# Kernel tuning notes

Measured on AMD Instinct MI355X. Metric: run time of the kernel, lower is better.

The kernel has to match this reference:

```python
import jax, jax.numpy as jnp
import numpy as np

N_HEAD = 16
NEG_BIG = 1e10  # matches the module's -10000000000.0 masking constant


def setup_inputs() -> dict:
    key = jax.random.key(0)
    k1, k2, k3 = jax.random.split(key, 3)
    B, S, D = 2, 2048, 1024
    std = 0.02
    return {
        "x": jax.random.normal(k1, (B, S, D), dtype=jnp.float32),
        "c_attn_w": jax.random.normal(k2, (D, 3 * D), dtype=jnp.float32) * std,
        "c_attn_b": jnp.zeros((3 * D,), dtype=jnp.float32),
        "c_proj_w": jax.random.normal(k3, (D, D), dtype=jnp.float32) * std,
        "c_proj_b": jnp.zeros((D,), dtype=jnp.float32),
    }


def reference(x, c_attn_w, c_attn_b, c_proj_w, c_proj_b):
    B, S, D = x.shape
    H = N_HEAD
    Dh = D // H

    # c_attn: fused QKV projection (Conv1D == linear)
    qkv = jnp.einsum("bsd,df->bsf", x, c_attn_w) + c_attn_b  # [B,S,3D]
    q, k, v = jnp.split(qkv, 3, axis=-1)

    def split_heads(t):  # [B,S,D] -> [B,H,S,Dh]
        return t.reshape(B, S, H, Dh).transpose(0, 2, 1, 3)

    q, k, v = split_heads(q), split_heads(k), split_heads(v)
    present = jnp.stack([k, v], axis=1)  # [B,2,H,S,Dh]

    # scores: explicit O(S^2) matrix, scaled by sqrt(head_dim)
    w = jnp.einsum("bhqd,bhkd->bhqk", q, k) / jnp.sqrt(
        jnp.asarray(Dh, dtype=q.dtype)
    )  # [B,H,S,S]

    # causal mask, applied exactly as in the source: w*mask - 1e10*(1-mask)
    mask = jnp.tril(jnp.ones((S, S), dtype=w.dtype))[None, None]  # [1,1,S,S]
    w = w * mask - NEG_BIG * (1.0 - mask)

    w = jax.nn.softmax(w, axis=-1)
    a = jnp.einsum("bhqk,bhkd->bhqd", w, v)  # [B,H,S,Dh]

    # merge heads: [B,H,S,Dh] -> [B,S,D]
    a = a.transpose(0, 2, 1, 3).reshape(B, S, D)

    # output projection
    a = jnp.einsum("bsd,df->bsf", a, c_proj_w) + c_proj_b
    return (a, present)
```

## Files before the change

kernel.cpp:

```cpp
#include <hip/hip_runtime.h>
#include <hip/hip_bf16.h>
#include <stdint.h>

typedef __bf16 bf16_t;
typedef __bf16 bf16x8 __attribute__((ext_vector_type(8)));
typedef __bf16 bf16x4v __attribute__((ext_vector_type(4)));
typedef float f32x4 __attribute__((ext_vector_type(4)));

#define MFMA16(A, B, C) __builtin_amdgcn_mfma_f32_16x16x32_bf16((A), (B), (C), 0, 0, 0)

#define BB 2
#define SS 2048
#define DD 1024
#define HH 16
#define DH 64
#define MM (BB * SS)

__device__ __forceinline__ void load_lds16(const void* g, void* l) {
  __builtin_amdgcn_global_load_lds(
      (const __attribute__((address_space(1))) void*)g,
      (__attribute__((address_space(3))) void*)l, 16, 0, 0);
}


__global__ __launch_bounds__(256) void cvt_f32_to_bf16(const float* __restrict__ in,
                                                       bf16_t* __restrict__ out, int n4) {
  int i = blockIdx.x * blockDim.x + threadIdx.x;
  if (i >= n4) return;
  float4 v = reinterpret_cast<const float4*>(in)[i];
  bf16x4v o;
  o[0] = (bf16_t)v.x; o[1] = (bf16_t)v.y; o[2] = (bf16_t)v.z; o[3] = (bf16_t)v.w;
  reinterpret_cast<bf16x4v*>(out)[i] = o;
}

__global__ void transpose_f32_to_bf16(const float* __restrict__ W, bf16_t* __restrict__ WT,
                                      int K, int N) {
  __shared__ float tile[32][33];
  int n0 = blockIdx.x * 32, k0 = blockIdx.y * 32;
  int tx = threadIdx.x, ty = threadIdx.y;
  #pragma unroll
  for (int i = ty; i < 32; i += 8) tile[i][tx] = W[(size_t)(k0 + i) * N + n0 + tx];
  __syncthreads();
  #pragma unroll
  for (int i = ty; i < 32; i += 8) WT[(size_t)(n0 + i) * K + k0 + tx] = (bf16_t)tile[tx][i];
}

template <int EPI>
__global__ __launch_bounds__(256) void gemm_bf16(
    const bf16_t* __restrict__ A, const bf16_t* __restrict__ BT,
    const float* __restrict__ bias, float* __restrict__ outf,
    bf16_t* __restrict__ q_b, bf16_t* __restrict__ k_b, bf16_t* __restrict__ vt_b,
    int M, int N, int K) {
  __shared__ __align__(16) bf16_t At[128 * 32];
  __shared__ __align__(16) bf16_t Bt[128 * 32];

  const int tid = threadIdx.x;
  const int l = tid & 63, w = tid >> 6;
  const int lr = l & 15, lg = l >> 4;
  const int wr = w >> 1, wc = w & 1;
  const int row0 = blockIdx.y * 128, col0 = blockIdx.x * 128;

  f32x4 vz = {0.f, 0.f, 0.f, 0.f};
  f32x4 acc[4][4];
  #pragma unroll
  for (int m = 0; m < 4; ++m)
    #pragma unroll
    for (int n = 0; n < 4; ++n) acc[m][n] = vz;

  for (int k0 = 0; k0 < K; k0 += 32) {
    __syncthreads();
    #pragma unroll
    for (int i = 0; i < 2; ++i) {
      int e = (tid + i * 256) * 8;
      int r = e >> 5, c = e & 31;
      int base = (w * 64 + i * 256) * 8;
      load_lds16(&A[(size_t)(row0 + r) * K + k0 + c], &At[base]);
      load_lds16(&BT[(size_t)(col0 + r) * K + k0 + c], &Bt[base]);
    }
    __syncthreads();
    bf16x8 af[4], bfr[4];
    #pragma unroll
    for (int m = 0; m < 4; ++m)
      af[m] = *(const bf16x8*)&At[(wr * 64 + m * 16 + lr) * 32 + lg * 8];
    #pragma unroll
    for (int n = 0; n < 4; ++n)
      bfr[n] = *(const bf16x8*)&Bt[(wc * 64 + n * 16 + lr) * 32 + lg * 8];
    #pragma unroll
    for (int m = 0; m < 4; ++m)
      #pragma unroll
      for (int n = 0; n < 4; ++n) acc[m][n] = MFMA16(af[m], bfr[n], acc[m][n]);
  }

  #pragma unroll
  for (int m = 0; m < 4; ++m) {
    int rl = wr * 64 + m * 16 + lg * 4;
    #pragma unroll
    for (int n = 0; n < 4; ++n) {
      int col = col0 + wc * 64 + n * 16 + lr;
      float bz = bias[col];
      #pragma unroll
      for (int r = 0; r < 4; ++r) {
        int row = row0 + rl + r;
        float v = acc[m][n][r] + bz;
        if (EPI == 1) {
          outf[(size_t)row * N + col] = v;
        } else {
          int b = row >> 11, s = row & 2047;
          int part = col >> 10, d = col & 1023;
          int h = d >> 6, dh = d & 63;
          size_t idx = ((size_t)(b * HH + h) * SS + s) * DH + dh;
          if (part == 0) {
            q_b[idx] = (bf16_t)v;
          } else if (part == 1) {
            k_b[idx] = (bf16_t)v;
            outf[(((size_t)(b * 2 + 0) * HH + h) * SS + s) * DH + dh] = v;
          } else {
            vt_b[((size_t)(b * HH + h) * DH + dh) * SS + s] = (bf16_t)v;
            outf[(((size_t)(b * 2 + 1) * HH + h) * SS + s) * DH + dh] = v;
          }
        }
      }
    }
  }
}

__global__ __launch_bounds__(256) void attn_fwd(
    const bf16_t* __restrict__ q_b, const bf16_t* __restrict__ k_b,
    const bf16_t* __restrict__ vt_b, bf16_t* __restrict__ attn_out) {
  __shared__ __align__(16) bf16_t Kt[64 * 64];
  __shared__ __align__(16) bf16_t Vt[64 * 64];
  __shared__ __align__(16) bf16_t P_lds[4][32][72];

  const int bh = blockIdx.y;
  const int q0b = (gridDim.x - 1 - blockIdx.x) * 128;
  const int tid = threadIdx.x;
  const int w = tid >> 6, l = tid & 63;
  const int lr = l & 15, lg = l >> 4;

  const bf16_t* qb = q_b + (size_t)bh * SS * DH;
  const bf16_t* kb = k_b + (size_t)bh * SS * DH;
  const bf16_t* vt = vt_b + (size_t)bh * DH * SS;

  const int qrow0 = q0b + w * 32 + lr;
  const int qrow1 = qrow0 + 16;
  bf16x8 qf[2][2];
  qf[0][0] = *(const bf16x8*)&qb[(size_t)qrow0 * DH + lg * 8];
  qf[0][1] = *(const bf16x8*)&qb[(size_t)qrow0 * DH + 32 + lg * 8];
  qf[1][0] = *(const bf16x8*)&qb[(size_t)qrow1 * DH + lg * 8];
  qf[1][1] = *(const bf16x8*)&qb[(size_t)qrow1 * DH + 32 + lg * 8];

  f32x4 vzero = {0.f, 0.f, 0.f, 0.f};
  f32x4 oacc[2][4];
  #pragma unroll
  for (int q = 0; q < 2; ++q)
    #pragma unroll
    for (int d = 0; d < 4; ++d) oacc[q][d] = vzero;
  float m_run[2] = {-1e30f, -1e30f}, l_run[2] = {0.f, 0.f};

  const int nkv = q0b / 64 + 2;
  for (int t = 0; t < nkv; ++t) {
    const int kv0 = t * 64;
    #pragma unroll
    for (int i = 0; i < 2; ++i) {
      int e = (tid + i * 256) * 8;
      int r = e >> 6;
      int cs = (((e & 63) * 2) ^ ((r & 7) << 4)) >> 1;
      int base = (w * 64 + i * 256) * 8;
      load_lds16(&kb[(size_t)(kv0 + r) * DH + cs], &Kt[base]);
      load_lds16(&vt[(size_t)r * SS + kv0 + cs], &Vt[base]);
    }
    __syncthreads();

    float sc[2][4][4];
    #pragma unroll
    for (int kvf = 0; kvf < 4; ++kvf) {
      int rr = kvf * 16 + lr;
      int sw = (rr & 7) << 4;
      bf16x8 kf0 = *(const bf16x8*)((const char*)Kt + rr * 128 + ((lg * 16) ^ sw));
      bf16x8 kf1 = *(const bf16x8*)((const char*)Kt + rr * 128 + ((64 + lg * 16) ^ sw));
      #pragma unroll
      for (int q = 0; q < 2; ++q) {
        f32x4 a = vzero;
        a = MFMA16(kf0, qf[q][0], a);
        a = MFMA16(kf1, qf[q][1], a);
        int qrow = q ? qrow1 : qrow0;
        #pragma unroll
        for (int r = 0; r < 4; ++r) {
          int kv = kv0 + kvf * 16 + lg * 4 + r;
          float s = a[r] * 0.125f;
          sc[q][kvf][r] = (kv > qrow) ? -1e10f : s;
        }
      }
    }

    #pragma unroll
    for (int q = 0; q < 2; ++q) {
      float tmax = -1e30f;
      #pragma unroll
      for (int kvf = 0; kvf < 4; ++kvf)
        #pragma unroll
        for (int r = 0; r < 4; ++r) tmax = fmaxf(tmax, sc[q][kvf][r]);
      tmax = fmaxf(tmax, __shfl_xor(tmax, 16));
      tmax = fmaxf(tmax, __shfl_xor(tmax, 32));
      float mnew = fmaxf(m_run[q], tmax);
      float alpha = __expf(m_run[q] - mnew);
      float psum = 0.f;
      #pragma unroll
      for (int kvf = 0; kvf < 4; ++kvf)
        #pragma unroll
        for (int r = 0; r < 4; ++r) {
          float p = __expf(sc[q][kvf][r] - mnew);
          sc[q][kvf][r] = p;
          psum += p;
        }
      psum += __shfl_xor(psum, 16);
      psum += __shfl_xor(psum, 32);
      l_run[q] = l_run[q] * alpha + psum;
      m_run[q] = mnew;
      #pragma unroll
      for (int d = 0; d < 4; ++d) oacc[q][d] *= alpha;
      #pragma unroll
      for (int kvf = 0; kvf < 4; ++kvf) {
        bf16x4v pk;
        #pragma unroll
        for (int r = 0; r < 4; ++r) pk[r] = (bf16_t)sc[q][kvf][r];
        *(bf16x4v*)&P_lds[w][q * 16 + lr][kvf * 16 + lg * 4] = pk;
      }
    }

    bf16x8 pf[2][2];
    #pragma unroll
    for (int q = 0; q < 2; ++q) {
      pf[q][0] = *(const bf16x8*)&P_lds[w][q * 16 + lr][lg * 8];
      pf[q][1] = *(const bf16x8*)&P_lds[w][q * 16 + lr][32 + lg * 8];
    }
    #pragma unroll
    for (int d = 0; d < 4; ++d) {
      int dl = d * 16 + lr;
      int sw = (dl & 7) << 4;
      bf16x8 vf0 = *(const bf16x8*)((const char*)Vt + dl * 128 + ((lg * 16) ^ sw));
      bf16x8 vf1 = *(const bf16x8*)((const char*)Vt + dl * 128 + ((64 + lg * 16) ^ sw));
      #pragma unroll
      for (int q = 0; q < 2; ++q) {
        oacc[q][d] = MFMA16(vf0, pf[q][0], oacc[q][d]);
        oacc[q][d] = MFMA16(vf1, pf[q][1], oacc[q][d]);
      }
    }
    __syncthreads();
  }

  const int b = bh >> 4, h = bh & 15;
  #pragma unroll
  for (int q = 0; q < 2; ++q) {
    float inv_l = 1.f / l_run[q];
    int qrow = q ? qrow1 : qrow0;
    #pragma unroll
    for (int d = 0; d < 4; ++d)
      #pragma unroll
      for (int r = 0; r < 4; ++r) {
        int dd = d * 16 + lg * 4 + r;
        attn_out[((size_t)(b * SS + qrow)) * DD + h * DH + dd] =
            (bf16_t)(oacc[q][d][r] * inv_l);
      }
  }
}

extern "C" void kernel_launch(void* const* d_in, const int* in_sizes, int n_in,
                              void* d_out, int out_size, void* d_ws, size_t ws_size,
                              hipStream_t stream) {
  const float* x = (const float*)d_in[0];
  const float* c_attn_w = (const float*)d_in[1];
  const float* c_attn_b = (const float*)d_in[2];
  const float* c_proj_w = (const float*)d_in[3];
  const float* c_proj_b = (const float*)d_in[4];

  float* out = (float*)d_out;
  float* present = out + (size_t)BB * SS * DD;

  char* ws = (char*)d_ws;
  bf16_t* xb     = (bf16_t*)(ws + 0);
  bf16_t* wqkvT  = (bf16_t*)(ws + 8388608);
  bf16_t* wprojT = (bf16_t*)(ws + 14680064);
  bf16_t* q_b    = (bf16_t*)(ws + 16777216);
  bf16_t* k_b    = (bf16_t*)(ws + 25165824);
  bf16_t* vt_b   = (bf16_t*)(ws + 33554432);
  bf16_t* attn_o = (bf16_t*)(ws + 41943040);

  cvt_f32_to_bf16<<<(MM * DD / 4 + 255) / 256, 256, 0, stream>>>(x, xb, MM * DD / 4);
  transpose_f32_to_bf16<<<dim3(3 * DD / 32, DD / 32), dim3(32, 8), 0, stream>>>(
      c_attn_w, wqkvT, DD, 3 * DD);
  transpose_f32_to_bf16<<<dim3(DD / 32, DD / 32), dim3(32, 8), 0, stream>>>(
      c_proj_w, wprojT, DD, DD);
  gemm_bf16<0><<<dim3(3 * DD / 128, MM / 128), 256, 0, stream>>>(
      xb, wqkvT, c_attn_b, present, q_b, k_b, vt_b, MM, 3 * DD, DD);
  attn_fwd<<<dim3(SS / 128, BB * HH), 256, 0, stream>>>(q_b, k_b, vt_b, attn_o);
  gemm_bf16<1><<<dim3(DD / 128, MM / 128), 256, 0, stream>>>(
      attn_o, wprojT, c_proj_b, out, nullptr, nullptr, nullptr, MM, DD, DD);
}
```

Measured before the change: 246.2 us.

## Double-buffer LDS tiles in GEMM and attention, skip masks and lazy softmax rescale

Both the GEMM and the attention kernel now use two LDS buffers, so the next K/V or A/B tile is fetched with global_load_lds while the current one is consumed. The aim is to hide global-load latency and drop one barrier per iteration. The attention kernel also applies the causal mask only on tiles that cross the diagonal, folds log2(e) into the score scale so it can use exp2f, and skips the running-max rescale when the max grows by at most 8. The lazy rescale can let exponentials reach up to 2^8, which costs some bf16 precision in P, and doubling LDS may lower occupancy.

```diff
diff --git a/kernel.cpp b/kernel.cpp
--- a/kernel.cpp
+++ b/kernel.cpp
@@ -51,8 +51,8 @@
     const float* __restrict__ bias, float* __restrict__ outf,
     bf16_t* __restrict__ q_b, bf16_t* __restrict__ k_b, bf16_t* __restrict__ vt_b,
     int M, int N, int K) {
-  __shared__ __align__(16) bf16_t At[128 * 32];
-  __shared__ __align__(16) bf16_t Bt[128 * 32];
+  __shared__ __align__(16) bf16_t At[2][128 * 32];
+  __shared__ __align__(16) bf16_t Bt[2][128 * 32];
 
   const int tid = threadIdx.x;
   const int l = tid & 63, w = tid >> 6;
@@ -60,35 +60,42 @@
   const int wr = w >> 1, wc = w & 1;
   const int row0 = blockIdx.y * 128, col0 = blockIdx.x * 128;
 
-  f32x4 vz = {0.f, 0.f, 0.f, 0.f};
-  f32x4 acc[4][4];
-  #pragma unroll
-  for (int m = 0; m < 4; ++m)
-    #pragma unroll
-    for (int n = 0; n < 4; ++n) acc[m][n] = vz;
-
-  for (int k0 = 0; k0 < K; k0 += 32) {
-    __syncthreads();
+  auto stage = [&](int buf, int k0) {
     #pragma unroll
     for (int i = 0; i < 2; ++i) {
       int e = (tid + i * 256) * 8;
       int r = e >> 5, c = e & 31;
       int base = (w * 64 + i * 256) * 8;
-      load_lds16(&A[(size_t)(row0 + r) * K + k0 + c], &At[base]);
-      load_lds16(&BT[(size_t)(col0 + r) * K + k0 + c], &Bt[base]);
-    }
+      load_lds16(&A[(size_t)(row0 + r) * K + k0 + c], &At[buf][base]);
+      load_lds16(&BT[(size_t)(col0 + r) * K + k0 + c], &Bt[buf][base]);
+    }
+  };
+
+  f32x4 vz = {0.f, 0.f, 0.f, 0.f};
+  f32x4 acc[4][4];
+  #pragma unroll
+  for (int m = 0; m < 4; ++m)
+    #pragma unroll
+    for (int n = 0; n < 4; ++n) acc[m][n] = vz;
+
+  stage(0, 0);
+  __syncthreads();
+  int cur = 0;
+  for (int k0 = 0; k0 < K; k0 += 32) {
+    if (k0 + 32 < K) stage(cur ^ 1, k0 + 32);
+    bf16x8 af[4], bfr[4];
+    #pragma unroll
+    for (int m = 0; m < 4; ++m)
+      af[m] = *(const bf16x8*)&At[cur][(wr * 64 + m * 16 + lr) * 32 + lg * 8];
+    #pragma unroll
+    for (int n = 0; n < 4; ++n)
+      bfr[n] = *(const bf16x8*)&Bt[cur][(wc * 64 + n * 16 + lr) * 32 + lg * 8];
+    #pragma unroll
+    for (int m = 0; m < 4; ++m)
+      #pragma unroll
+      for (int n = 0; n < 4; ++n) acc[m][n] = MFMA16(af[m], bfr[n], acc[m][n]);
     __syncthreads();
-    bf16x8 af[4], bfr[4];
-    #pragma unroll
-    for (int m = 0; m < 4; ++m)
-      af[m] = *(const bf16x8*)&At[(wr * 64 + m * 16 + lr) * 32 + lg * 8];
-    #pragma unroll
-    for (int n = 0; n < 4; ++n)
-      bfr[n] = *(const bf16x8*)&Bt[(wc * 64 + n * 16 + lr) * 32 + lg * 8];
-    #pragma unroll
-    for (int m = 0; m < 4; ++m)
-      #pragma unroll
-      for (int n = 0; n < 4; ++n) acc[m][n] = MFMA16(af[m], bfr[n], acc[m][n]);
+    cur ^= 1;
   }
 
   #pragma unroll
@@ -127,8 +134,8 @@
 __global__ __launch_bounds__(256) void attn_fwd(
     const bf16_t* __restrict__ q_b, const bf16_t* __restrict__ k_b,
     const bf16_t* __restrict__ vt_b, bf16_t* __restrict__ attn_out) {
-  __shared__ __align__(16) bf16_t Kt[64 * 64];
-  __shared__ __align__(16) bf16_t Vt[64 * 64];
+  __shared__ __align__(16) bf16_t Kt[2][64 * 64];
+  __shared__ __align__(16) bf16_t Vt[2][64 * 64];
   __shared__ __align__(16) bf16_t P_lds[4][32][72];
 
   const int bh = blockIdx.y;
@@ -140,6 +147,18 @@
   const bf16_t* qb = q_b + (size_t)bh * SS * DH;
   const bf16_t* kb = k_b + (size_t)bh * SS * DH;
   const bf16_t* vt = vt_b + (size_t)bh * DH * SS;
+
+  auto stageKV = [&](int buf, int kv0) {
+    #pragma unroll
+    for (int i = 0; i < 2; ++i) {
+      int e = (tid + i * 256) * 8;
+      int r = e >> 6;
+      int cs = (((e & 63) * 2) ^ ((r & 7) << 4)) >> 1;
+      int base = (w * 64 + i * 256) * 8;
+      load_lds16(&kb[(size_t)(kv0 + r) * DH + cs], &Kt[buf][base]);
+      load_lds16(&vt[(size_t)r * SS + kv0 + cs], &Vt[buf][base]);
+    }
+  };
 
   const int qrow0 = q0b + w * 32 + lr;
   const int qrow1 = qrow0 + 16;
@@ -157,39 +176,44 @@
     for (int d = 0; d < 4; ++d) oacc[q][d] = vzero;
   float m_run[2] = {-1e30f, -1e30f}, l_run[2] = {0.f, 0.f};
 
+  const float SCL = 0.125f * 1.4426950408889634f;
+
   const int nkv = q0b / 64 + 2;
+  stageKV(0, 0);
+  __syncthreads();
+  int cur = 0;
   for (int t = 0; t < nkv; ++t) {
     const int kv0 = t * 64;
-    #pragma unroll
-    for (int i = 0; i < 2; ++i) {
-      int e = (tid + i * 256) * 8;
-      int r = e >> 6;
-      int cs = (((e & 63) * 2) ^ ((r & 7) << 4)) >> 1;
-      int base = (w * 64 + i * 256) * 8;
-      load_lds16(&kb[(size_t)(kv0 + r) * DH + cs], &Kt[base]);
-      load_lds16(&vt[(size_t)r * SS + kv0 + cs], &Vt[base]);
-    }
-    __syncthreads();
+    if (t + 1 < nkv) stageKV(cur ^ 1, (t + 1) * 64);
 
     float sc[2][4][4];
     #pragma unroll
     for (int kvf = 0; kvf < 4; ++kvf) {
       int rr = kvf * 16 + lr;
       int sw = (rr & 7) << 4;
-      bf16x8 kf0 = *(const bf16x8*)((const char*)Kt + rr * 128 + ((lg * 16) ^ sw));
-      bf16x8 kf1 = *(const bf16x8*)((const char*)Kt + rr * 128 + ((64 + lg * 16) ^ sw));
+      const char* kbase = (const char*)&Kt[cur][0] + rr * 128;
+      bf16x8 kf0 = *(const bf16x8*)(kbase + ((lg * 16) ^ sw));
+      bf16x8 kf1 = *(const bf16x8*)(kbase + ((64 + lg * 16) ^ sw));
       #pragma unroll
       for (int q = 0; q < 2; ++q) {
         f32x4 a = vzero;
         a = MFMA16(kf0, qf[q][0], a);
         a = MFMA16(kf1, qf[q][1], a);
+        #pragma unroll
+        for (int r = 0; r < 4; ++r) sc[q][kvf][r] = a[r] * SCL;
+      }
+    }
+    if (kv0 + 63 > q0b + w * 32) {
+      #pragma unroll
+      for (int q = 0; q < 2; ++q) {
         int qrow = q ? qrow1 : qrow0;
         #pragma unroll
-        for (int r = 0; r < 4; ++r) {
-          int kv = kv0 + kvf * 16 + lg * 4 + r;
-          float s = a[r] * 0.125f;
-          sc[q][kvf][r] = (kv > qrow) ? -1e10f : s;
-        }
+        for (int kvf = 0; kvf < 4; ++kvf)
+          #pragma unroll
+          for (int r = 0; r < 4; ++r) {
+            int kv = kv0 + kvf * 16 + lg * 4 + r;
+            if (kv > qrow) sc[q][kvf][r] = -3.0e9f;
+          }
       }
     }
 
@@ -202,23 +226,27 @@
         for (int r = 0; r < 4; ++r) tmax = fmaxf(tmax, sc[q][kvf][r]);
       tmax = fmaxf(tmax, __shfl_xor(tmax, 16));
       tmax = fmaxf(tmax, __shfl_xor(tmax, 32));
-      float mnew = fmaxf(m_run[q], tmax);
-      float alpha = __expf(m_run[q] - mnew);
+      if (!__all(tmax <= m_run[q] + 8.0f)) {
+        float mnew = fmaxf(m_run[q], tmax);
+        float alpha = exp2f(m_run[q] - mnew);
+        l_run[q] *= alpha;
+        #pragma unroll
+        for (int d = 0; d < 4; ++d) oacc[q][d] *= alpha;
+        m_run[q] = mnew;
+      }
+      float mq = m_run[q];
       float psum = 0.f;
       #pragma unroll
       for (int kvf = 0; kvf < 4; ++kvf)
         #pragma unroll
         for (int r = 0; r < 4; ++r) {
-          float p = __expf(sc[q][kvf][r] - mnew);
+          float p = exp2f(sc[q][kvf][r] - mq);
           sc[q][kvf][r] = p;
           psum += p;
         }
       psum += __shfl_xor(psum, 16);
       psum += __shfl_xor(psum, 32);
-      l_run[q] = l_run[q] * alpha + psum;
-      m_run[q] = mnew;
-      #pragma unroll
-      for (int d = 0; d < 4; ++d) oacc[q][d] *= alpha;
+      l_run[q] += psum;
       #pragma unroll
       for (int kvf = 0; kvf < 4; ++kvf) {
         bf16x4v pk;
@@ -238,8 +266,9 @@
     for (int d = 0; d < 4; ++d) {
       int dl = d * 16 + lr;
       int sw = (dl & 7) << 4;
-      bf16x8 vf0 = *(const bf16x8*)((const char*)Vt + dl * 128 + ((lg * 16) ^ sw));
-      bf16x8 vf1 = *(const bf16x8*)((const char*)Vt + dl * 128 + ((64 + lg * 16) ^ sw));
+      const char* vbase = (const char*)&Vt[cur][0] + dl * 128;
+      bf16x8 vf0 = *(const bf16x8*)(vbase + ((lg * 16) ^ sw));
+      bf16x8 vf1 = *(const bf16x8*)(vbase + ((64 + lg * 16) ^ sw));
       #pragma unroll
       for (int q = 0; q < 2; ++q) {
         oacc[q][d] = MFMA16(vf0, pf[q][0], oacc[q][d]);
@@ -247,6 +276,7 @@
       }
     }
     __syncthreads();
+    cur ^= 1;
   }
 
   const int b = bh >> 4, h = bh & 15;
```

Measured after the change: 245.4 us. About the same (-0.3%).
